# Kernel optimization log

Measured on AMD Instinct MI355X. Metric: run time of the kernel, lower is better.

## Reference

```python
import jax, jax.numpy as jnp
import numpy as np

N_NODES, N_EDGES, D, N_MOVIE, N_GENRE, L_MAX = 50000, 400000, 128, 20400, 30, 680
HOPS, HEADS, C_HEAD, N_LAYERS, T_HEADS, FF = 3, 4, 32, 4, 4, 2048


def _leaky(x, s):
    return jnp.where(x >= 0, x, s * x)


def _layer_norm(x, g, b, eps=1e-5):
    m = x.mean(-1, keepdims=True)
    v = ((x - m) ** 2).mean(-1, keepdims=True)
    return (x - m) / jnp.sqrt(v + eps) * g + b


def _gat_conv(x, ei, W, a_src, a_dst, b):
    # PyG GATConv: add self-loops, per-head linear, edge-softmax over incoming edges.
    N = x.shape[0]
    loop = jnp.arange(N)
    src = jnp.concatenate([ei[0], loop])
    dst = jnp.concatenate([ei[1], loop])
    h = (x @ W.T).reshape(N, HEADS, C_HEAD)
    al_s = (h * a_src[None]).sum(-1)  # [N, H]
    al_d = (h * a_dst[None]).sum(-1)
    e = _leaky(al_s[src] + al_d[dst], 0.2)  # [E+N, H]
    m = jax.ops.segment_max(e, dst, num_segments=N)
    ee = jnp.exp(e - m[dst])
    den = jax.ops.segment_sum(ee, dst, num_segments=N)
    alpha = ee / den[dst]
    out = jax.ops.segment_sum(h[src] * alpha[:, :, None], dst, num_segments=N)
    return out.reshape(N, HEADS * C_HEAD) + b


def _mha(y, pad_mask, qkv_w, qkv_b, out_w, out_b):
    B, S, Dm = y.shape
    hd = Dm // T_HEADS
    qkv = y @ qkv_w.T + qkv_b
    q, k, v = jnp.split(qkv, 3, axis=-1)
    q = q.reshape(B, S, T_HEADS, hd).transpose(0, 2, 1, 3)
    k = k.reshape(B, S, T_HEADS, hd).transpose(0, 2, 1, 3)
    v = v.reshape(B, S, T_HEADS, hd).transpose(0, 2, 1, 3)
    scores = jnp.einsum('bhqd,bhkd->bhqk', q, k) / jnp.sqrt(jnp.float32(hd))
    scores = jnp.where(pad_mask[:, None, None, :], -1e9, scores)
    a = jax.nn.softmax(scores, axis=-1)
    o = jnp.einsum('bhqk,bhkd->bhqd', a, v).transpose(0, 2, 1, 3).reshape(B, S, Dm)
    return o @ out_w.T + out_b


def _forward(x, e0, e1, e2, movie_idx, genre, gat_W, gat_att_src, gat_att_dst, gat_bias,
             dec_W, dec_b, qkv_w, qkv_b, out_w, out_b, ln1_g, ln1_b, ln2_g, ln2_b,
             ffn_w1, ffn_b1, ffn_w2, ffn_b2, fus_w, fus_b):
    edges = [e0, e1, e2]
    acc = jnp.zeros_like(x)
    for kk in range(HOPS):  # multi-hop GAT with exp hop decay (dropout off: eval)
        h = _gat_conv(x, edges[kk], gat_W[kk], gat_att_src[kk], gat_att_dst[kk], gat_bias[kk])
        h = _leaky(h @ dec_W[kk].T + dec_b[kk], 0.01)
        acc = acc + float(np.exp(-0.1 * kk)) * h
    x = acc
    xm = x[movie_idx]  # x[genre_mask]
    # group movie nodes into padded per-genre sequences [N_GENRE, L_MAX, D]
    onehot = jax.nn.one_hot(genre, N_GENRE, dtype=jnp.int32)
    pos = jnp.cumsum(onehot, axis=0)[jnp.arange(genre.shape[0]), genre] - 1
    counts = jnp.sum(onehot, axis=0)
    all_genre = jnp.zeros((N_GENRE, L_MAX, x.shape[1]), x.dtype).at[genre, pos].set(xm)
    pad_mask = jnp.arange(L_MAX)[None, :] >= counts[:, None]  # True = padding
    y = all_genre
    for l in range(N_LAYERS):  # PyTorch post-LN TransformerEncoder, relu FFN, eval dropout
        a = _mha(y, pad_mask, qkv_w[l], qkv_b[l], out_w[l], out_b[l])
        y = _layer_norm(y + a, ln1_g[l], ln1_b[l])
        f = jax.nn.relu(y @ ffn_w1[l].T + ffn_b1[l]) @ ffn_w2[l].T + ffn_b2[l]
        y = _layer_norm(y + f, ln2_g[l], ln2_b[l])
    # genre_backward: mean-pool per genre, gather back per node
    valid = (~pad_mask).astype(x.dtype)
    pooled = (y * valid[..., None]).sum(1) / jnp.maximum(valid.sum(1), 1.0)[:, None]
    emb = pooled[genre]
    fused = _leaky(jnp.concatenate([xm, emb], axis=1) @ fus_w.T + fus_b, 0.01)
    return x.at[movie_idx].set(fused)


def setup_inputs() -> dict:
    key = jax.random.key(0)
    ks = jax.random.split(key, 24)
    s = 0.05
    nrm = lambda i, shp: jax.random.normal(ks[i], shp, jnp.float32) * s
    return {
        'x': jax.random.normal(ks[0], (N_NODES, D), jnp.float32),
        'edge_index_hop0': jax.random.randint(ks[1], (2, N_EDGES), 0, N_NODES),
        'edge_index_hop1': jax.random.randint(ks[2], (2, N_EDGES), 0, N_NODES),
        'edge_index_hop2': jax.random.randint(ks[3], (2, N_EDGES), 0, N_NODES),
        'movie_idx': jnp.arange(N_MOVIE),
        'genre': jnp.arange(N_MOVIE) % N_GENRE,
        'gat_W': nrm(4, (HOPS, D, D)),
        'gat_att_src': nrm(5, (HOPS, HEADS, C_HEAD)),
        'gat_att_dst': nrm(6, (HOPS, HEADS, C_HEAD)),
        'gat_bias': nrm(7, (HOPS, D)),
        'dec_W': nrm(8, (HOPS, D, D)),
        'dec_b': nrm(9, (HOPS, D)),
        'qkv_w': nrm(10, (N_LAYERS, 3 * D, D)),
        'qkv_b': nrm(11, (N_LAYERS, 3 * D)),
        'out_w': nrm(12, (N_LAYERS, D, D)),
        'out_b': nrm(13, (N_LAYERS, D)),
        'ln1_g': jnp.ones((N_LAYERS, D), jnp.float32),
        'ln1_b': jnp.zeros((N_LAYERS, D), jnp.float32),
        'ln2_g': jnp.ones((N_LAYERS, D), jnp.float32),
        'ln2_b': jnp.zeros((N_LAYERS, D), jnp.float32),
        'ffn_w1': nrm(14, (N_LAYERS, FF, D)),
        'ffn_b1': nrm(15, (N_LAYERS, FF)),
        'ffn_w2': nrm(16, (N_LAYERS, D, FF)),
        'ffn_b2': nrm(17, (N_LAYERS, D)),
        'fus_w': nrm(18, (D, 2 * D)),
        'fus_b': nrm(19, (D,)),
    }


def reference(x, edge_index_hop0, edge_index_hop1, edge_index_hop2, movie_idx, genre,
              gat_W, gat_att_src, gat_att_dst, gat_bias, dec_W, dec_b,
              qkv_w, qkv_b, out_w, out_b, ln1_g, ln1_b, ln2_g, ln2_b,
              ffn_w1, ffn_b1, ffn_w2, ffn_b2, fus_w, fus_b):
    return _forward(x, edge_index_hop0, edge_index_hop1, edge_index_hop2, movie_idx, genre,
                    gat_W, gat_att_src, gat_att_dst, gat_bias, dec_W, dec_b,
                    qkv_w, qkv_b, out_w, out_b, ln1_g, ln1_b, ln2_g, ln2_b,
                    ffn_w1, ffn_b1, ffn_w2, ffn_b2, fus_w, fus_b)
```

## Files before the change

### kernel.cpp

```cpp
#include <hip/hip_runtime.h>

#define N_NODES  50000
#define N_EDGES  400000
#define DIM      128
#define N_MOVIE  20400
#define N_GENRE  30
#define L_MAX    680
#define NROWS    (N_GENRE * L_MAX)
#define FF       2048
#define N_LAYERS 4

#define NBKT 98
#define NPB  512
#define ECAP 4608
#define SCAP 5120
#define EPGB (NBKT * ECAP)
#define SPGB (NBKT * SCAP)

typedef __attribute__((ext_vector_type(8))) short bf16x8;
typedef __attribute__((ext_vector_type(4))) float f32x4;

#define MFMA16 __builtin_amdgcn_mfma_f32_16x16x32_bf16

__device__ __forceinline__ float b2f(ushort u) {
    union { unsigned i; float f; } c; c.i = ((unsigned)u) << 16; return c.f;
}
__device__ __forceinline__ ushort f2b(float f) {
    union { float f; unsigned i; } c; c.f = f;
    unsigned u = c.i;
    u += 0x7FFFu + ((u >> 16) & 1u);
    return (ushort)(u >> 16);
}
__device__ __forceinline__ bf16x8 load8s(const ushort* p) {
    return *(const bf16x8*)p;
}
__device__ __forceinline__ void async16(const ushort* g, ushort* l) {
    __builtin_amdgcn_global_load_lds(
        (const __attribute__((address_space(1))) void*)g,
        (__attribute__((address_space(3))) void*)l, 16, 0, 0);
}

__device__ __forceinline__ void cvt8(const float* s, ushort* d, int i) {
    const float4* q = (const float4*)(s + (size_t)i * 8);
    float4 a = q[0], b = q[1];
    bf16x8 r;
    r[0] = (short)f2b(a.x); r[1] = (short)f2b(a.y);
    r[2] = (short)f2b(a.z); r[3] = (short)f2b(a.w);
    r[4] = (short)f2b(b.x); r[5] = (short)f2b(b.y);
    r[6] = (short)f2b(b.z); r[7] = (short)f2b(b.w);
    *(bf16x8*)(d + (size_t)i * 8) = r;
}

__global__ void cvt32(const float* __restrict__ s, ushort* __restrict__ d, int n8)
{
    int i = blockIdx.x * blockDim.x + threadIdx.x;
    if (i < n8) cvt8(s, d, i);
}

__global__ void cvt_w(const float* gatW, const float* decW, const float* qkvW,
                      const float* outW, const float* fw1, const float* fw2,
                      const float* fusW,
                      ushort* gatWb, ushort* decWb, ushort* qkvWb,
                      ushort* outWb, ushort* fw1b, ushort* fw2b, ushort* fusWb)
{
    const float* s; ushort* d; int n8;
    switch (blockIdx.y) {
        case 0: s = gatW; d = gatWb; n8 = 49152 / 8; break;
        case 1: s = decW; d = decWb; n8 = 49152 / 8; break;
        case 2: s = qkvW; d = qkvWb; n8 = 196608 / 8; break;
        case 3: s = outW; d = outWb; n8 = 65536 / 8; break;
        case 4: s = fw1;  d = fw1b;  n8 = 1048576 / 8; break;
        case 5: s = fw2;  d = fw2b;  n8 = 1048576 / 8; break;
        default: s = fusW; d = fusWb; n8 = 32768 / 8; break;
    }
    int i = blockIdx.x * 256 + threadIdx.x;
    if (i < n8) cvt8(s, d, i);
}

template<int BM, int ACT, int EPI, int OBF>
__global__ __launch_bounds__(256) void gemm_lds(
    const ushort* __restrict__ A, const ushort* __restrict__ W,
    const float* __restrict__ bias, void* __restrict__ Cv,
    int M, int N, int K, float scale)
{
    __shared__ ushort smem[BM * 128 + 128 * 128];
    ushort* As = smem;
    ushort* Ws = smem + BM * 128;
    const int tid  = threadIdx.x;
    const int wave = tid >> 6, lane = tid & 63;
    const int quad = lane >> 4, l16 = lane & 15;
    const int m0 = blockIdx.x * BM;
    const int n0 = blockIdx.y * 128;

    constexpr int MT = BM / 32;
    const int mbase = (wave & 1) * (BM / 2);
    const int nbase = (wave >> 1) * 64;

    f32x4 acc[MT][4] = {};
    for (int k0 = 0; k0 < K; k0 += 128) {
        if (k0) __syncthreads();
#pragma unroll
        for (int i = 0; i < BM / 16; i++) {
            int seg = i * 256 + tid;
            int r = seg >> 4, s = seg & 15;
            int rg = min(m0 + r, M - 1);
            async16(A + (size_t)rg * K + k0 + ((s ^ (r & 15)) * 8),
                    As + r * 128 + s * 8);
        }
#pragma unroll
        for (int i = 0; i < 8; i++) {
            int seg = i * 256 + tid;
            int r = seg >> 4, s = seg & 15;
            async16(W + (size_t)(n0 + r) * K + k0 + ((s ^ (r & 15)) * 8),
                    Ws + r * 128 + s * 8);
        }
        __syncthreads();

#pragma unroll
        for (int kk = 0; kk < 4; kk++) {
            bf16x8 a[MT], b[4];
#pragma unroll
            for (int mt = 0; mt < MT; mt++)
                a[mt] = load8s(As + (mbase + mt * 16 + l16) * 128 +
                               (((kk * 4 + quad) ^ l16) * 8));
#pragma unroll
            for (int nt = 0; nt < 4; nt++)
                b[nt] = load8s(Ws + (nbase + nt * 16 + l16) * 128 +
                               (((kk * 4 + quad) ^ l16) * 8));
#pragma unroll
            for (int mt = 0; mt < MT; mt++)
#pragma unroll
                for (int nt = 0; nt < 4; nt++)
                    acc[mt][nt] = MFMA16(a[mt], b[nt], acc[mt][nt], 0, 0, 0);
        }
    }

    if constexpr (OBF == 1) {
        static_assert(BM == 128, "OBF=1 staged epilogue assumes BM=128");
        ushort* Cs = smem;
        __syncthreads();
#pragma unroll
        for (int p = 0; p < 2; p++) {
            if ((wave & 1) == p) {
#pragma unroll
                for (int nt = 0; nt < 4; nt++) {
                    const int col = nbase + nt * 16 + l16;
                    const float bv = bias ? bias[n0 + col] : 0.f;
#pragma unroll
                    for (int mt = 0; mt < MT; mt++) {
                        const int rl = mt * 16 + quad * 4;
#pragma unroll
                        for (int r = 0; r < 4; r++) {
                            float v = acc[mt][nt][r] + bv;
                            if (ACT == 1) v = (v >= 0.f) ? v : 0.01f * v;
                            if (ACT == 2) v = fmaxf(v, 0.f);
                            Cs[(rl + r) * 128 + col] = f2b(v);
                        }
                    }
                }
            }
            __syncthreads();
            const int row = tid >> 2, cb = (tid & 3) * 32;
            const int grow = m0 + p * 64 + row;
            if (grow < M) {
                const ushort* s = Cs + row * 128 + cb;
                ushort* dp = (ushort*)Cv + (size_t)grow * N + n0 + cb;
                *(int4*)(dp)      = *(const int4*)(s);
                *(int4*)(dp + 8)  = *(const int4*)(s + 8);
                *(int4*)(dp + 16) = *(const int4*)(s + 16);
                *(int4*)(dp + 24) = *(const int4*)(s + 24);
            }
            __syncthreads();
        }
    } else {
#pragma unroll
        for (int nt = 0; nt < 4; nt++) {
            const int col = n0 + nbase + nt * 16 + l16;
            const float bv = bias ? bias[col] : 0.f;
#pragma unroll
            for (int mt = 0; mt < MT; mt++) {
                if (OBF == 2) {
                    const int row0 = m0 + mbase + mt * 16 + quad * 4;
                    if (row0 < M) {
                        ushort4 pk;
                        pk.x = f2b(acc[mt][nt][0] + bv);
                        pk.y = f2b(acc[mt][nt][1] + bv);
                        pk.z = f2b(acc[mt][nt][2] + bv);
                        pk.w = f2b(acc[mt][nt][3] + bv);
                        *(ushort4*)((ushort*)Cv + (size_t)col * M + row0) = pk;
                    }
                } else {
#pragma unroll
                    for (int r = 0; r < 4; r++) {
                        const int row = m0 + mbase + mt * 16 + quad * 4 + r;
                        if (row < M) {
                            float v = acc[mt][nt][r] + bv;
                            if (ACT == 1) v = (v >= 0.f) ? v : 0.01f * v;
                            if (ACT == 2) v = fmaxf(v, 0.f);
                            const size_t idx = (size_t)row * N + col;
                            if (EPI == 1) ((float*)Cv)[idx] += scale * v;
                            else          ((float*)Cv)[idx] = v;
                        }
                    }
                }
            }
        }
    }
}

__global__ __launch_bounds__(256, 2) void ffn_fused(
    const ushort* __restrict__ y, const ushort* __restrict__ w1,
    const float* __restrict__ b1, const ushort* __restrict__ w2,
    const float* __restrict__ b2,
    float* __restrict__ o0, float* __restrict__ o1,
    float* __restrict__ o2, float* __restrict__ o3, int M)
{
    __shared__ ushort f1s[2][32 * 128];
    __shared__ ushort f2s[2][128 * 32];
    __shared__ ushort mids[4][32 * 40];

    const int tid  = threadIdx.x;
    const int wave = tid >> 6, lane = tid & 63;
    const int quad = lane >> 4, l16 = lane & 15;
    const int m0 = blockIdx.x * 128;
    const int fh = blockIdx.y;
    const int fbase = fh * (FF / 4);
    float* o = (fh == 0) ? o0 : (fh == 1) ? o1 : (fh == 2) ? o2 : o3;

    const int sw1 = ((tid & 15) ^ (tid >> 4)) * 8;
    const int sw2 = ((tid & 3) ^ ((tid >> 3) & 3)) * 8;

    const int wrow = m0 + wave * 32;
    bf16x8 yf[2][4];
#pragma unroll
    for (int mt = 0; mt < 2; mt++) {
        const int mr = min(wrow + mt * 16 + l16, M - 1);
#pragma unroll
        for (int ks = 0; ks < 4; ks++)
            yf[mt][ks] = load8s(y + (size_t)mr * 128 + ks * 32 + quad * 8);
    }

#pragma unroll
    for (int i = 0; i < 2; i++) {
        int row = i * 16 + (tid >> 4);
        async16(w1 + (size_t)(fbase + row) * 128 + sw1,
                f1s[0] + row * 128 + (tid & 15) * 8);
    }
#pragma unroll
    for (int i = 0; i < 2; i++) {
        int row = i * 64 + (tid >> 2);
        async16(w2 + (size_t)row * FF + fbase + sw2,
                f2s[0] + row * 32 + (tid & 3) * 8);
    }

    f32x4 oacc[2][8] = {};
    ushort* midw = mids[wave];
    int cur = 0;
    __syncthreads();

    for (int fo = 0; fo < FF / 4; fo += 32) {
        if (fo + 32 < FF / 4) {
            const int fn = fbase + fo + 32;
#pragma unroll
            for (int i = 0; i < 2; i++) {
                int row = i * 16 + (tid >> 4);
                async16(w1 + (size_t)(fn + row) * 128 + sw1,
                        f1s[cur ^ 1] + row * 128 + (tid & 15) * 8);
            }
#pragma unroll
            for (int i = 0; i < 2; i++) {
                int row = i * 64 + (tid >> 2);
                async16(w2 + (size_t)row * FF + fn + sw2,
                        f2s[cur ^ 1] + row * 32 + (tid & 3) * 8);
            }
        }
        const ushort* F1 = f1s[cur];
        const ushort* F2 = f2s[cur];

        f32x4 midacc[2][2] = {};
#pragma unroll
        for (int ks = 0; ks < 4; ks++) {
            const int csA = (((ks * 4 + quad) ^ l16) & 15) * 8;
#pragma unroll
            for (int ft = 0; ft < 2; ft++) {
                bf16x8 wf = load8s(F1 + (ft * 16 + l16) * 128 + csA);
                midacc[0][ft] = MFMA16(wf, yf[0][ks], midacc[0][ft], 0, 0, 0);
                midacc[1][ft] = MFMA16(wf, yf[1][ks], midacc[1][ft], 0, 0, 0);
            }
        }
#pragma unroll
        for (int mt = 0; mt < 2; mt++)
#pragma unroll
            for (int ft = 0; ft < 2; ft++) {
                const float4 bb = *(const float4*)(b1 + fbase + fo + ft * 16 + quad * 4);
                ushort4 pk;
                pk.x = f2b(fmaxf(midacc[mt][ft][0] + bb.x, 0.f));
                pk.y = f2b(fmaxf(midacc[mt][ft][1] + bb.y, 0.f));
                pk.z = f2b(fmaxf(midacc[mt][ft][2] + bb.z, 0.f));
                pk.w = f2b(fmaxf(midacc[mt][ft][3] + bb.w, 0.f));
                *(ushort4*)(midw + (mt * 16 + l16) * 40 + ft * 16 + quad * 4) = pk;
            }
        bf16x8 mf0 = load8s(midw + (size_t)l16 * 40 + quad * 8);
        bf16x8 mf1 = load8s(midw + (size_t)(16 + l16) * 40 + quad * 8);
        const int gB = (quad ^ ((l16 >> 1) & 3)) * 8;
#pragma unroll
        for (int dt = 0; dt < 8; dt++) {
            bf16x8 wf = load8s(F2 + (dt * 16 + l16) * 32 + gB);
            oacc[0][dt] = MFMA16(wf, mf0, oacc[0][dt], 0, 0, 0);
            oacc[1][dt] = MFMA16(wf, mf1, oacc[1][dt], 0, 0, 0);
        }
        __syncthreads();
        cur ^= 1;
    }

#pragma unroll
    for (int mt = 0; mt < 2; mt++) {
        const int m = wrow + mt * 16 + l16;
        if (m < M) {
            float* op = o + (size_t)m * 128 + quad * 4;
#pragma unroll
            for (int dt = 0; dt < 8; dt++) {
                float4 v;
                if (fh == 0) {
                    const float4 bv = *(const float4*)(b2 + dt * 16 + quad * 4);
                    v.x = oacc[mt][dt][0] + bv.x;
                    v.y = oacc[mt][dt][1] + bv.y;
                    v.z = oacc[mt][dt][2] + bv.z;
                    v.w = oacc[mt][dt][3] + bv.w;
                } else {
                    v.x = oacc[mt][dt][0];
                    v.y = oacc[mt][dt][1];
                    v.z = oacc[mt][dt][2];
                    v.w = oacc[mt][dt][3];
                }
                *(float4*)(op + dt * 16) = v;
            }
        }
    }
}

__global__ void gat_al(const ushort* __restrict__ h,
                       const float* __restrict__ asrc, const float* __restrict__ adst,
                       float* __restrict__ als, float* __restrict__ ald, int N)
{
    int idx = blockIdx.x * blockDim.x + threadIdx.x;
    if (idx >= N * 4) return;
    int n = idx >> 2, hh = idx & 3;
    const ushort* hp = h + (size_t)n * DIM + hh * 32;
    float s = 0.f, d = 0.f;
#pragma unroll
    for (int q = 0; q < 4; q++) {
        bf16x8 hv = load8s(hp + q * 8);
#pragma unroll
        for (int c = 0; c < 8; c++) {
            float v = b2f((ushort)hv[c]);
            s += v * asrc[hh * 32 + q * 8 + c];
            d += v * adst[hh * 32 + q * 8 + c];
        }
    }
    als[idx] = s; ald[idx] = d;
}

__global__ void csr_initb(int* __restrict__ bcur)
{
    int i = blockIdx.x * 256 + threadIdx.x;
    if (i < 3 * NBKT) bcur[i * 16] = (i % NBKT) * ECAP;
}

__global__ __launch_bounds__(256) void csr_route(
    const int* __restrict__ e0, const int* __restrict__ e1, const int* __restrict__ e2,
    int* __restrict__ bcur, int* __restrict__ ebuf)
{
    __shared__ int hist[NBKT], base[NBKT], cur[NBKT];
    const int g = blockIdx.y, t = threadIdx.x;
    const int* e = (g == 0) ? e0 : (g == 1) ? e1 : e2;
    const int i0 = blockIdx.x * 4096;
    for (int j = t; j < NBKT; j += 256) { hist[j] = 0; cur[j] = 0; }
    __syncthreads();
    unsigned pk[16]; int bk[16];
#pragma unroll
    for (int j = 0; j < 16; j++) {
        int i = i0 + j * 256 + t;
        if (i < N_EDGES) {
            int s = e[i], d = e[N_EDGES + i];
            bk[j] = d >> 9;
            pk[j] = (unsigned)s | ((unsigned)(d & 511) << 16);
            atomicAdd(&hist[bk[j]], 1);
        } else bk[j] = -1;
    }
    __syncthreads();
    for (int j = t; j < NBKT; j += 256)
        if (hist[j]) base[j] = atomicAdd(&bcur[(g * NBKT + j) * 16], hist[j]);
    __syncthreads();
#pragma unroll
    for (int j = 0; j < 16; j++)
        if (bk[j] >= 0) {
            int p = base[bk[j]] + atomicAdd(&cur[bk[j]], 1);
            ebuf[(size_t)g * EPGB + p] = (int)pk[j];
        }
}

__global__ __launch_bounds__(256) void csr_build(
    const int* __restrict__ bcur, const int* __restrict__ ebuf,
    int* __restrict__ off, int* __restrict__ deg, int* __restrict__ srcs)
{
    __shared__ int hist[NPB];
    __shared__ int part[256];
    const int g = blockIdx.y, b = blockIdx.x, t = threadIdx.x;
    const int nb0 = b * NPB;
    const int nn = min(NPB, N_NODES - nb0);
    const int cnt = bcur[(g * NBKT + b) * 16] - b * ECAP;
    const int* eb = ebuf + (size_t)g * EPGB + b * ECAP;

    for (int j = t; j < NPB; j += 256) hist[j] = (j < nn) ? 1 : 0;
    __syncthreads();
    for (int i = t; i < cnt; i += 256)
        atomicAdd(&hist[(eb[i] >> 16) & 511], 1);
    __syncthreads();

    int a0 = hist[t * 2], a1 = hist[t * 2 + 1];
    int sum = a0 + a1;
    part[t] = sum;
    __syncthreads();
    for (int d = 1; d < 256; d <<= 1) {
        int x = (t >= d) ? part[t - d] : 0;
        __syncthreads();
        part[t] += x;
        __syncthreads();
    }
    const int excl = part[t] - sum;
    __syncthreads();
    const int sb = b * SCAP;
    hist[t * 2]     = excl;
    hist[t * 2 + 1] = excl + a0;
    if (t * 2 < nn) {
        off[(size_t)g * N_NODES + nb0 + t * 2] = sb + excl;
        deg[(size_t)g * N_NODES + nb0 + t * 2] = a0;
    }
    if (t * 2 + 1 < nn) {
        off[(size_t)g * N_NODES + nb0 + t * 2 + 1] = sb + excl + a0;
        deg[(size_t)g * N_NODES + nb0 + t * 2 + 1] = a1;
    }
    __syncthreads();

    int* sg = srcs + (size_t)g * SPGB + sb;
    for (int i = t; i < cnt; i += 256) {
        int v = eb[i];
        int p = atomicAdd(&hist[(v >> 16) & 511], 1);
        sg[p] = v & 0xFFFF;
    }
    for (int j = t; j < nn; j += 256) {
        int p = atomicAdd(&hist[j], 1);
        sg[p] = nb0 + j;
    }
}

__global__ __launch_bounds__(256) void gat_gather(
    const int* __restrict__ off, const int* __restrict__ deg, const int* __restrict__ srcs,
    const ushort* __restrict__ hb, const float* __restrict__ als,
    const float* __restrict__ ald, const float* __restrict__ bias,
    ushort* __restrict__ ob)
{
    int w = (blockIdx.x * 256 + threadIdx.x) >> 6;
    int lane = threadIdx.x & 63;
    if (w >= N_NODES) return;
    const int grp  = lane >> 4;
    const int l16  = lane & 15;
    const int head = l16 >> 2;
    const float adv = ald[(size_t)w * 4 + head];
    const int jb = off[w], dg = deg[w];

    float acc[8] = {};
    float wsum = 0.f;

    int j = grp;
    int s = (j < dg) ? srcs[jb + j] : 0;
    while (j < dg) {
        const int jn = j + 4;
        const int sn = (jn < dg) ? srcs[jb + jn] : 0;
        bf16x8 hv = load8s(hb + (size_t)s * DIM + l16 * 8);
        float e = als[(size_t)s * 4 + head] + adv;
        e = (e >= 0.f) ? e : 0.2f * e;
        const float wg = __expf(e);
        wsum += wg;
#pragma unroll
        for (int c = 0; c < 8; c++) acc[c] += wg * b2f((ushort)hv[c]);
        j = jn; s = sn;
    }

    wsum += __shfl_xor(wsum, 16, 64);
    wsum += __shfl_xor(wsum, 32, 64);
#pragma unroll
    for (int c = 0; c < 8; c++) {
        acc[c] += __shfl_xor(acc[c], 16, 64);
        acc[c] += __shfl_xor(acc[c], 32, 64);
    }

    if (grp == 0) {
        const float inv = 1.f / wsum;
        bf16x8 r;
#pragma unroll
        for (int c = 0; c < 8; c++)
            r[c] = (short)f2b(acc[c] * inv + bias[l16 * 8 + c]);
        *(bf16x8*)(ob + (size_t)w * DIM + l16 * 8) = r;
    }
}

__global__ void calc_pos(const int* __restrict__ genre, int* __restrict__ pos,
                         int* __restrict__ cnt, int NM)
{
    int i = blockIdx.x * blockDim.x + threadIdx.x;
    if (i < NM) pos[i] = atomicAdd(&cnt[genre[i]], 1);
}

__global__ void build_y(const float* __restrict__ acc, const int* __restrict__ midx,
                        const int* __restrict__ genre, const int* __restrict__ pos,
                        float* __restrict__ y, ushort* __restrict__ yb)
{
    int i = blockIdx.x, c = threadIdx.x;
    int g = genre[i], p = pos[i];
    float v = acc[(size_t)midx[i] * DIM + c];
    size_t o = ((size_t)g * L_MAX + p) * DIM + c;
    y[o] = v; yb[o] = f2b(v);
}

#define SP 40

__global__ __launch_bounds__(256) void flash_attn(
    const ushort* __restrict__ qk, const ushort* __restrict__ vtg,
    const int* __restrict__ cnt, ushort* __restrict__ o)
{
    __shared__ ushort Pb[4][32 * SP];

    const int qt = blockIdx.x, hh = blockIdx.y, g = blockIdx.z;
    const int t = threadIdx.x, wave = t >> 6, lane = t & 63;
    const int quad = lane >> 4, l16 = lane & 15;
    const int L = cnt[g];
    const float scale = 0.17677669529663687f;
    const ushort* base = qk + (size_t)g * L_MAX * 256;
    const ushort* vb0 = vtg + (size_t)(hh * 32 + l16) * NROWS + g * L_MAX;
    const ushort* vb1 = vb0 + (size_t)16 * NROWS;

    const int q0 = qt * 128 + wave * 32;
    bf16x8 a0 = load8s(base + (size_t)min(q0 + l16,      L_MAX - 1) * 256 + hh * 32 + quad * 8);
    bf16x8 a1 = load8s(base + (size_t)min(q0 + 16 + l16, L_MAX - 1) * 256 + hh * 32 + quad * 8);

    f32x4 oacc[2][2] = {};
    float rsum[2] = {0.f, 0.f};
    ushort* P = Pb[wave];

    for (int kt = 0; kt < 704; kt += 32) {
        bf16x8 b0 = load8s(base + (size_t)min(kt + l16,      L_MAX - 1) * 256 + 128 + hh * 32 + quad * 8);
        bf16x8 b1 = load8s(base + (size_t)min(kt + 16 + l16, L_MAX - 1) * 256 + 128 + hh * 32 + quad * 8);
        f32x4 z = {};
        f32x4 st00 = MFMA16(b0, a0, z, 0, 0, 0);
        f32x4 st01 = MFMA16(b0, a1, z, 0, 0, 0);
        f32x4 st10 = MFMA16(b1, a0, z, 0, 0, 0);
        f32x4 st11 = MFMA16(b1, a1, z, 0, 0, 0);

        const int kc0 = kt + quad * 4, kc1 = kt + 16 + quad * 4;
#pragma unroll
        for (int qh = 0; qh < 2; qh++) {
            const f32x4 sA = qh ? st01 : st00;
            const f32x4 sB = qh ? st11 : st10;
            float w[8];
#pragma unroll
            for (int r = 0; r < 4; r++) {
                w[r]     = (kc0 + r < L) ? __expf(sA[r] * scale) : 0.f;
                w[4 + r] = (kc1 + r < L) ? __expf(sB[r] * scale) : 0.f;
                rsum[qh] += w[r] + w[4 + r];
            }
            ushort4 pk0, pk1;
            pk0.x = f2b(w[0]); pk0.y = f2b(w[1]); pk0.z = f2b(w[2]); pk0.w = f2b(w[3]);
            pk1.x = f2b(w[4]); pk1.y = f2b(w[5]); pk1.z = f2b(w[6]); pk1.w = f2b(w[7]);
            *(ushort4*)(P + (qh * 16 + l16) * SP + quad * 4)      = pk0;
            *(ushort4*)(P + (qh * 16 + l16) * SP + 16 + quad * 4) = pk1;
        }
        bf16x8 p0 = load8s(P + (size_t)l16 * SP + quad * 8);
        bf16x8 p1 = load8s(P + (size_t)(16 + l16) * SP + quad * 8);
        bf16x8 v0 = load8s(vb0 + kt + quad * 8);
        bf16x8 v1 = load8s(vb1 + kt + quad * 8);
        oacc[0][0] = MFMA16(v0, p0, oacc[0][0], 0, 0, 0);
        oacc[0][1] = MFMA16(v0, p1, oacc[0][1], 0, 0, 0);
        oacc[1][0] = MFMA16(v1, p0, oacc[1][0], 0, 0, 0);
        oacc[1][1] = MFMA16(v1, p1, oacc[1][1], 0, 0, 0);
    }

#pragma unroll
    for (int qh = 0; qh < 2; qh++) {
        float s = rsum[qh];
        s += __shfl_xor(s, 16, 64);
        s += __shfl_xor(s, 32, 64);
        const int q = q0 + qh * 16 + l16;
        if (q < L_MAX) {
            const float inv = 1.f / s;
#pragma unroll
            for (int dh = 0; dh < 2; dh++) {
                ushort4 pk;
                pk.x = f2b(oacc[dh][qh][0] * inv);
                pk.y = f2b(oacc[dh][qh][1] * inv);
                pk.z = f2b(oacc[dh][qh][2] * inv);
                pk.w = f2b(oacc[dh][qh][3] * inv);
                *(ushort4*)(o + ((size_t)(g * L_MAX + q)) * DIM + hh * 32 + dh * 16 + quad * 4) = pk;
            }
        }
    }
}

__global__ __launch_bounds__(256) void ln_res(
    float* __restrict__ y, const float* __restrict__ res,
    const float* __restrict__ res2, const float* __restrict__ res3,
    const float* __restrict__ res4,
    const float* __restrict__ g, const float* __restrict__ b,
    ushort* __restrict__ yb)
{
    const int r = blockIdx.x * 4 + (threadIdx.x >> 6);
    const int lane = threadIdx.x & 63;
    const size_t base = (size_t)r * DIM + lane * 2;
    float2 v = *(const float2*)(y + base);
    {
        float2 a = *(const float2*)(res + base);
        v.x += a.x; v.y += a.y;
    }
    if (res2) {
        float2 a = *(const float2*)(res2 + base);
        v.x += a.x; v.y += a.y;
    }
    if (res3) {
        float2 a = *(const float2*)(res3 + base);
        float2 c = *(const float2*)(res4 + base);
        v.x += a.x + c.x; v.y += a.y + c.y;
    }
    float s = v.x + v.y;
#pragma unroll
    for (int off = 32; off; off >>= 1) s += __shfl_xor(s, off, 64);
    const float mean = s * (1.f / 128.f);
    const float dx = v.x - mean, dy = v.y - mean;
    float q = dx * dx + dy * dy;
#pragma unroll
    for (int off = 32; off; off >>= 1) q += __shfl_xor(q, off, 64);
    const float rst = rsqrtf(q * (1.f / 128.f) + 1e-5f);
    const float2 gg = *(const float2*)(g + lane * 2);
    const float2 bb = *(const float2*)(b + lane * 2);
    float2 ov;
    ov.x = dx * rst * gg.x + bb.x;
    ov.y = dy * rst * gg.y + bb.y;
    *(float2*)(y + base) = ov;
    ushort2 pk;
    pk.x = f2b(ov.x);
    pk.y = f2b(ov.y);
    *(ushort2*)(yb + base) = pk;
}

__global__ __launch_bounds__(256) void pool_partial(
    const float* __restrict__ y, const int* __restrict__ cnt, float* __restrict__ pooled)
{
    __shared__ float sh[128];
    const int g = blockIdx.x, seg = blockIdx.y, t = threadIdx.x;
    const int c = t & 127, h = t >> 7;
    const int L = cnt[g];
    const int k0 = seg * 40, k1 = min(k0 + 40, L);
    float s = 0.f;
    for (int k = k0 + h; k < k1; k += 2) s += y[((size_t)g * L_MAX + k) * DIM + c];
    if (h) sh[c] = s;
    __syncthreads();
    if (!h) {
        float tot = s + sh[c];
        if (k0 < L) atomicAdd(&pooled[g * DIM + c], tot / (float)max(L, 1));
    }
}

__global__ void build_fin(const float* __restrict__ acc, const float* __restrict__ pooled,
                          const int* __restrict__ midx, const int* __restrict__ genre,
                          ushort* __restrict__ A2)
{
    const int i = blockIdx.x, t = threadIdx.x;
    float v = (t < 128) ? acc[(size_t)midx[i] * DIM + t]
                        : pooled[genre[i] * DIM + (t - 128)];
    A2[(size_t)i * 256 + t] = f2b(v);
}

__global__ void scatter_movies(const float* __restrict__ fused, const int* __restrict__ midx,
                               float* __restrict__ out)
{
    const int i = blockIdx.x, c = threadIdx.x;
    out[(size_t)midx[i] * DIM + c] = fused[(size_t)i * DIM + c];
}

extern "C" void kernel_launch(void* const* d_in, const int* in_sizes, int n_in,
                              void* d_out, int out_size, void* d_ws, size_t ws_size,
                              hipStream_t stream)
{
    const float* x      = (const float*)d_in[0];
    const int* e[3]     = { (const int*)d_in[1], (const int*)d_in[2], (const int*)d_in[3] };
    const int* midx     = (const int*)d_in[4];
    const int* genre    = (const int*)d_in[5];
    const float* gatW   = (const float*)d_in[6];
    const float* attS   = (const float*)d_in[7];
    const float* attD   = (const float*)d_in[8];
    const float* gatB   = (const float*)d_in[9];
    const float* decW   = (const float*)d_in[10];
    const float* decB   = (const float*)d_in[11];
    const float* qkvW   = (const float*)d_in[12];
    const float* qkvB   = (const float*)d_in[13];
    const float* outW   = (const float*)d_in[14];
    const float* outB   = (const float*)d_in[15];
    const float* ln1g   = (const float*)d_in[16];
    const float* ln1b   = (const float*)d_in[17];
    const float* ln2g   = (const float*)d_in[18];
    const float* ln2b   = (const float*)d_in[19];
    const float* fw1    = (const float*)d_in[20];
    const float* fb1    = (const float*)d_in[21];
    const float* fw2    = (const float*)d_in[22];
    const float* fb2    = (const float*)d_in[23];
    const float* fusW   = (const float*)d_in[24];
    const float* fusB   = (const float*)d_in[25];
    float* out = (float*)d_out;

    float* ws  = (float*)d_ws;
    float* acc = ws;
    float* R   = ws + 6400000;
    ushort* xb   = (ushort*)(R);
    ushort* hb   = (ushort*)(R + 3200000);
    ushort* gbx  = (ushort*)(R + 6400000);
    float*  als  = R + 9600000;
    float*  ald  = R + 9800000;
    int*   bcur  = (int*)(R + 10000000);
    int*   ebuf  = (int*)(R + 10004736);
    int*   off3  = (int*)(R + 11359488);
    int*   deg3  = (int*)(R + 11509488);
    int*   srcs3 = (int*)(R + 11659488);
    ushort* gatWb= (ushort*)(R + 13164768);
    ushort* decWb= (ushort*)(R + 13189344);
    float*  ybuf  = R;
    float*  tmp   = R + 2611200;
    ushort* ybx   = (ushort*)(R + 5222400);
    ushort* attnb = (ushort*)(R + 6528000);
    ushort* qkvb  = (ushort*)(R + 7833600);
    ushort* vtg   = (ushort*)(R + 10444800);
    ushort* finb  = (ushort*)(R + 11750400);
    float*  tmp2  = R + 14361600;
    float*  tmp3  = R + 16972800;
    float*  tmp4  = R + 19584000;
    float*  pooled= R + 22195200;
    int*    cntb  = (int*)(R + 22199040);
    int*    posb  = cntb + 32;
    ushort* qkvWb = (ushort*)(R + 22220000);
    ushort* outWb = (ushort*)(R + 22318304);
    ushort* fw1b  = (ushort*)(R + 22351072);
    ushort* fw2b  = (ushort*)(R + 22875360);
    ushort* fusWb = (ushort*)(R + 23399648);

    const float decay[3] = { 1.0f, 0.90483741803595952f, 0.81873075307798182f };

    cvt_w<<<dim3(512, 7), 256, 0, stream>>>(
        gatW, decW, qkvW, outW, fw1, fw2, fusW,
        gatWb, decWb, qkvWb, outWb, fw1b, fw2b, fusWb);
    cvt32<<<(6400000 / 8 + 255) / 256, 256, 0, stream>>>(x, xb, 6400000 / 8);

    csr_initb<<<(3 * NBKT + 255) / 256, 256, 0, stream>>>(bcur);
    csr_route<<<dim3((N_EDGES + 4095) / 4096, 3), 256, 0, stream>>>(
        e[0], e[1], e[2], bcur, ebuf);
    csr_build<<<dim3(NBKT, 3), 256, 0, stream>>>(bcur, ebuf, off3, deg3, srcs3);

    for (int k = 0; k < 3; k++) {
        gemm_lds<128, 0, 0, 1><<<dim3(391, 1), 256, 0, stream>>>(
            xb, gatWb + k * DIM * DIM, nullptr, hb, N_NODES, DIM, DIM, 1.f);
        gat_al<<<(N_NODES * 4 + 255) / 256, 256, 0, stream>>>(
            hb, attS + k * DIM, attD + k * DIM, als, ald, N_NODES);
        gat_gather<<<(N_NODES * 64 + 255) / 256, 256, 0, stream>>>(
            off3 + (size_t)k * N_NODES, deg3 + (size_t)k * N_NODES,
            srcs3 + (size_t)k * SPGB, hb, als, ald, gatB + k * DIM, gbx);
        if (k == 0)
            gemm_lds<128, 1, 0, 0><<<dim3(391, 1), 256, 0, stream>>>(
                gbx, decWb, decB, acc, N_NODES, DIM, DIM, 1.f);
        else
            gemm_lds<128, 1, 1, 0><<<dim3(391, 1), 256, 0, stream>>>(
                gbx, decWb + k * DIM * DIM, decB + k * DIM, acc, N_NODES, DIM, DIM, decay[k]);
    }

    hipMemsetAsync(cntb, 0, 32 * 4, stream);
    calc_pos<<<(N_MOVIE + 255) / 256, 256, 0, stream>>>(genre, posb, cntb, N_MOVIE);
    build_y<<<N_MOVIE, 128, 0, stream>>>(acc, midx, genre, posb, ybuf, ybx);

    for (int l = 0; l < N_LAYERS; l++) {
        gemm_lds<128, 0, 0, 1><<<dim3(160, 2), 256, 0, stream>>>(
            ybx, qkvWb + (size_t)l * 384 * DIM, qkvB + l * 384, qkvb, NROWS, 256, DIM, 1.f);
        gemm_lds<128, 0, 0, 2><<<dim3(160, 1), 256, 0, stream>>>(
            ybx, qkvWb + (size_t)l * 384 * DIM + 256 * DIM, qkvB + l * 384 + 256,
            vtg, NROWS, DIM, DIM, 1.f);
        flash_attn<<<dim3(6, 4, 30), 256, 0, stream>>>(qkvb, vtg, cntb, attnb);
        gemm_lds<64, 0, 0, 0><<<dim3(319, 1), 256, 0, stream>>>(
            attnb, outWb + (size_t)l * DIM * DIM, outB + l * DIM, tmp, NROWS, DIM, DIM, 1.f);
        ln_res<<<NROWS / 4, 256, 0, stream>>>(ybuf, tmp, nullptr, nullptr, nullptr,
                                              ln1g + l * DIM, ln1b + l * DIM, ybx);
        ffn_fused<<<dim3((NROWS + 127) / 128, 4), 256, 0, stream>>>(
            ybx, fw1b + (size_t)l * FF * DIM, fb1 + (size_t)l * FF,
            fw2b + (size_t)l * DIM * FF, fb2 + (size_t)l * DIM,
            tmp, tmp2, tmp3, tmp4, NROWS);
        ln_res<<<NROWS / 4, 256, 0, stream>>>(ybuf, tmp, tmp2, tmp3, tmp4,
                                              ln2g + l * DIM, ln2b + l * DIM, ybx);
    }

    hipMemsetAsync(pooled, 0, 3840 * 4, stream);
    pool_partial<<<dim3(N_GENRE, 17), 256, 0, stream>>>(ybuf, cntb, pooled);
    build_fin<<<N_MOVIE, 256, 0, stream>>>(acc, pooled, midx, genre, finb);
    gemm_lds<64, 1, 0, 0><<<dim3(319, 1), 256, 0, stream>>>(
        finb, fusWb, fusB, tmp, NROWS, DIM, 256, 1.f);

    hipMemcpyAsync(out, acc, (size_t)6400000 * 4, hipMemcpyDeviceToDevice, stream);
    scatter_movies<<<N_MOVIE, 128, 0, stream>>>(tmp, midx, out);
}
```

Before: 922.5 us.

## Batch GAT hops across grid z, fuse QKV GEMMs, accumulate directly into output

The three GAT hops' projection GEMM, attention-logit and gather kernels now each run as one launch indexed by blockIdx, with per-hop buffers, so small kernels fill the GPU better and launch count drops. The separate QK and V GEMMs become a single qkv_gemm launch with three column blocks. The accumulator is written straight into the output buffer, removing a 25.6MB device-to-device copy. The cost is larger workspace for per-hop buffers, and the final scatter now depends on acc aliasing out.

Result: faster. 867.0 us (-6.0%).

```diff
diff --git a/kernel.cpp b/kernel.cpp
--- a/kernel.cpp
+++ b/kernel.cpp
@@ -79,9 +79,9 @@
 
 template<int BM, int ACT, int EPI, int OBF>
 __global__ __launch_bounds__(256) void gemm_lds(
-    const ushort* __restrict__ A, const ushort* __restrict__ W,
+    const ushort* __restrict__ A, const ushort* __restrict__ W_,
     const float* __restrict__ bias, void* __restrict__ Cv,
-    int M, int N, int K, float scale)
+    int M, int N, int K, float scale, size_t wstride, size_t cstride)
 {
     __shared__ ushort smem[BM * 128 + 128 * 128];
     ushort* As = smem;
@@ -91,6 +91,8 @@
     const int quad = lane >> 4, l16 = lane & 15;
     const int m0 = blockIdx.x * BM;
     const int n0 = blockIdx.y * 128;
+    const int hop = blockIdx.z;
+    const ushort* W = W_ + (size_t)hop * wstride;
 
     constexpr int MT = BM / 32;
     const int mbase = (wave & 1) * (BM / 2);
@@ -164,7 +166,8 @@
             const int grow = m0 + p * 64 + row;
             if (grow < M) {
                 const ushort* s = Cs + row * 128 + cb;
-                ushort* dp = (ushort*)Cv + (size_t)grow * N + n0 + cb;
+                ushort* dp = (ushort*)Cv + (size_t)hop * cstride +
+                             (size_t)grow * N + n0 + cb;
                 *(int4*)(dp)      = *(const int4*)(s);
                 *(int4*)(dp + 8)  = *(const int4*)(s + 8);
                 *(int4*)(dp + 16) = *(const int4*)(s + 16);
@@ -179,29 +182,120 @@
             const float bv = bias ? bias[col] : 0.f;
 #pragma unroll
             for (int mt = 0; mt < MT; mt++) {
-                if (OBF == 2) {
-                    const int row0 = m0 + mbase + mt * 16 + quad * 4;
-                    if (row0 < M) {
-                        ushort4 pk;
-                        pk.x = f2b(acc[mt][nt][0] + bv);
-                        pk.y = f2b(acc[mt][nt][1] + bv);
-                        pk.z = f2b(acc[mt][nt][2] + bv);
-                        pk.w = f2b(acc[mt][nt][3] + bv);
-                        *(ushort4*)((ushort*)Cv + (size_t)col * M + row0) = pk;
+#pragma unroll
+                for (int r = 0; r < 4; r++) {
+                    const int row = m0 + mbase + mt * 16 + quad * 4 + r;
+                    if (row < M) {
+                        float v = acc[mt][nt][r] + bv;
+                        if (ACT == 1) v = (v >= 0.f) ? v : 0.01f * v;
+                        if (ACT == 2) v = fmaxf(v, 0.f);
+                        const size_t idx = (size_t)row * N + col;
+                        if (EPI == 1) ((float*)Cv)[idx] += scale * v;
+                        else          ((float*)Cv)[idx] = v;
                     }
-                } else {
-#pragma unroll
-                    for (int r = 0; r < 4; r++) {
-                        const int row = m0 + mbase + mt * 16 + quad * 4 + r;
-                        if (row < M) {
-                            float v = acc[mt][nt][r] + bv;
-                            if (ACT == 1) v = (v >= 0.f) ? v : 0.01f * v;
-                            if (ACT == 2) v = fmaxf(v, 0.f);
-                            const size_t idx = (size_t)row * N + col;
-                            if (EPI == 1) ((float*)Cv)[idx] += scale * v;
-                            else          ((float*)Cv)[idx] = v;
-                        }
+                }
+            }
+        }
+    }
+}
+
+__global__ __launch_bounds__(256) void qkv_gemm(
+    const ushort* __restrict__ A, const ushort* __restrict__ W0,
+    const float* __restrict__ bias0, ushort* __restrict__ qkv,
+    ushort* __restrict__ vt, int M)
+{
+    __shared__ ushort smem[2 * 128 * 128];
+    ushort* As = smem;
+    ushort* Ws = smem + 128 * 128;
+    const int tid  = threadIdx.x;
+    const int wave = tid >> 6, lane = tid & 63;
+    const int quad = lane >> 4, l16 = lane & 15;
+    const int m0 = blockIdx.x * 128;
+    const int sel = blockIdx.y;
+    const ushort* W = W0 + (size_t)sel * 128 * 128;
+    const int mbase = (wave & 1) * 64;
+    const int nbase = (wave >> 1) * 64;
+
+    f32x4 acc[4][4] = {};
+#pragma unroll
+    for (int i = 0; i < 8; i++) {
+        int seg = i * 256 + tid;
+        int r = seg >> 4, s = seg & 15;
+        int rg = min(m0 + r, M - 1);
+        async16(A + (size_t)rg * 128 + ((s ^ (r & 15)) * 8), As + r * 128 + s * 8);
+    }
+#pragma unroll
+    for (int i = 0; i < 8; i++) {
+        int seg = i * 256 + tid;
+        int r = seg >> 4, s = seg & 15;
+        async16(W + (size_t)r * 128 + ((s ^ (r & 15)) * 8), Ws + r * 128 + s * 8);
+    }
+    __syncthreads();
+#pragma unroll
+    for (int kk = 0; kk < 4; kk++) {
+        bf16x8 a[4], b[4];
+#pragma unroll
+        for (int mt = 0; mt < 4; mt++)
+            a[mt] = load8s(As + (mbase + mt * 16 + l16) * 128 +
+                           (((kk * 4 + quad) ^ l16) * 8));
+#pragma unroll
+        for (int nt = 0; nt < 4; nt++)
+            b[nt] = load8s(Ws + (nbase + nt * 16 + l16) * 128 +
+                           (((kk * 4 + quad) ^ l16) * 8));
+#pragma unroll
+        for (int mt = 0; mt < 4; mt++)
+#pragma unroll
+            for (int nt = 0; nt < 4; nt++)
+                acc[mt][nt] = MFMA16(a[mt], b[nt], acc[mt][nt], 0, 0, 0);
+    }
+
+    if (sel < 2) {
+        ushort* Cs = smem;
+        __syncthreads();
+#pragma unroll
+        for (int p = 0; p < 2; p++) {
+            if ((wave & 1) == p) {
+#pragma unroll
+                for (int nt = 0; nt < 4; nt++) {
+                    const int col = nbase + nt * 16 + l16;
+                    const float bv = bias0[sel * 128 + col];
+#pragma unroll
+                    for (int mt = 0; mt < 4; mt++) {
+                        const int rl = mt * 16 + quad * 4;
+#pragma unroll
+                        for (int r = 0; r < 4; r++)
+                            Cs[(rl + r) * 128 + col] = f2b(acc[mt][nt][r] + bv);
                     }
+                }
+            }
+            __syncthreads();
+            const int row = tid >> 2, cb = (tid & 3) * 32;
+            const int grow = m0 + p * 64 + row;
+            if (grow < M) {
+                const ushort* s = Cs + row * 128 + cb;
+                ushort* dp = qkv + (size_t)grow * 256 + sel * 128 + cb;
+                *(int4*)(dp)      = *(const int4*)(s);
+                *(int4*)(dp + 8)  = *(const int4*)(s + 8);
+                *(int4*)(dp + 16) = *(const int4*)(s + 16);
+                *(int4*)(dp + 24) = *(const int4*)(s + 24);
+            }
+            __syncthreads();
+        }
+    } else {
+#pragma unroll
+        for (int nt = 0; nt < 4; nt++) {
+            const int col = nbase + nt * 16 + l16;
+            const float bv = bias0[256 + col];
+#pragma unroll
+            for (int mt = 0; mt < 4; mt++) {
+                const int row0 = m0 + mbase + mt * 16 + quad * 4;
+                if (row0 < M) {
+                    ushort4 pk;
+                    pk.x = f2b(acc[mt][nt][0] + bv);
+                    pk.y = f2b(acc[mt][nt][1] + bv);
+                    pk.z = f2b(acc[mt][nt][2] + bv);
+                    pk.w = f2b(acc[mt][nt][3] + bv);
+                    *(ushort4*)(vt + (size_t)col * M + row0) = pk;
                 }
             }
         }
@@ -218,7 +312,6 @@
     __shared__ ushort f1s[2][32 * 128];
     __shared__ ushort f2s[2][128 * 32];
     __shared__ ushort mids[4][32 * 40];
-
     const int tid  = threadIdx.x;
     const int wave = tid >> 6, lane = tid & 63;
     const int quad = lane >> 4, l16 = lane & 15;
@@ -339,12 +432,16 @@
     }
 }
 
-__global__ void gat_al(const ushort* __restrict__ h,
+__global__ void gat_al(const ushort* __restrict__ hb3,
                        const float* __restrict__ asrc, const float* __restrict__ adst,
-                       float* __restrict__ als, float* __restrict__ ald, int N)
+                       float* __restrict__ als3, float* __restrict__ ald3, int N)
 {
     int idx = blockIdx.x * blockDim.x + threadIdx.x;
     if (idx >= N * 4) return;
+    const int hop = blockIdx.y;
+    const ushort* h = hb3 + (size_t)hop * N * DIM;
+    const float* as_ = asrc + hop * DIM;
+    const float* ad_ = adst + hop * DIM;
     int n = idx >> 2, hh = idx & 3;
     const ushort* hp = h + (size_t)n * DIM + hh * 32;
     float s = 0.f, d = 0.f;
@@ -354,11 +451,12 @@
 #pragma unroll
         for (int c = 0; c < 8; c++) {
             float v = b2f((ushort)hv[c]);
-            s += v * asrc[hh * 32 + q * 8 + c];
-            d += v * adst[hh * 32 + q * 8 + c];
-        }
-    }
-    als[idx] = s; ald[idx] = d;
+            s += v * as_[hh * 32 + q * 8 + c];
+            d += v * ad_[hh * 32 + q * 8 + c];
+        }
+    }
+    als3[(size_t)hop * N * 4 + idx] = s;
+    ald3[(size_t)hop * N * 4 + idx] = d;
 }
 
 __global__ void csr_initb(int* __restrict__ bcur)
@@ -456,14 +554,24 @@
 }
 
 __global__ __launch_bounds__(256) void gat_gather(
-    const int* __restrict__ off, const int* __restrict__ deg, const int* __restrict__ srcs,
-    const ushort* __restrict__ hb, const float* __restrict__ als,
-    const float* __restrict__ ald, const float* __restrict__ bias,
-    ushort* __restrict__ ob)
+    const int* __restrict__ off3, const int* __restrict__ deg3,
+    const int* __restrict__ srcs3, const ushort* __restrict__ hb3,
+    const float* __restrict__ als3, const float* __restrict__ ald3,
+    const float* __restrict__ bias3, ushort* __restrict__ gbx3)
 {
     int w = (blockIdx.x * 256 + threadIdx.x) >> 6;
     int lane = threadIdx.x & 63;
     if (w >= N_NODES) return;
+    const int hop = blockIdx.y;
+    const int* off = off3 + (size_t)hop * N_NODES;
+    const int* deg = deg3 + (size_t)hop * N_NODES;
+    const int* srcs = srcs3 + (size_t)hop * SPGB;
+    const ushort* hb = hb3 + (size_t)hop * N_NODES * DIM;
+    const float* als = als3 + (size_t)hop * N_NODES * 4;
+    const float* ald = ald3 + (size_t)hop * N_NODES * 4;
+    const float* bias = bias3 + hop * DIM;
+    ushort* ob = gbx3 + (size_t)hop * N_NODES * DIM;
+
     const int grp  = lane >> 4;
     const int l16  = lane & 15;
     const int head = l16 >> 2;
@@ -718,20 +826,20 @@
     float* out = (float*)d_out;
 
     float* ws  = (float*)d_ws;
-    float* acc = ws;
+    float* acc = out;
     float* R   = ws + 6400000;
-    ushort* xb   = (ushort*)(R);
-    ushort* hb   = (ushort*)(R + 3200000);
-    ushort* gbx  = (ushort*)(R + 6400000);
-    float*  als  = R + 9600000;
-    float*  ald  = R + 9800000;
-    int*   bcur  = (int*)(R + 10000000);
-    int*   ebuf  = (int*)(R + 10004736);
-    int*   off3  = (int*)(R + 11359488);
-    int*   deg3  = (int*)(R + 11509488);
-    int*   srcs3 = (int*)(R + 11659488);
-    ushort* gatWb= (ushort*)(R + 13164768);
-    ushort* decWb= (ushort*)(R + 13189344);
+    ushort* xb   = (ushort*)(ws);
+    ushort* gatWb= (ushort*)(ws + 3200000);
+    ushort* decWb= (ushort*)(ws + 3224576);
+    float*  als3 = ws + 3249152;
+    float*  ald3 = ws + 3849152;
+    int*    off3 = (int*)(ws + 4449152);
+    int*    deg3 = (int*)(ws + 4599152);
+    ushort* hb3  = (ushort*)(R);
+    ushort* gbx3 = (ushort*)(R + 9600000);
+    int*   bcur  = (int*)(R + 19200000);
+    int*   ebuf  = (int*)(R + 19204736);
+    int*   srcs3 = (int*)(R + 20559488);
     float*  ybuf  = R;
     float*  tmp   = R + 2611200;
     ushort* ybx   = (ushort*)(R + 5222400);
@@ -763,20 +871,21 @@
         e[0], e[1], e[2], bcur, ebuf);
     csr_build<<<dim3(NBKT, 3), 256, 0, stream>>>(bcur, ebuf, off3, deg3, srcs3);
 
+    gemm_lds<128, 0, 0, 1><<<dim3(391, 1, 3), 256, 0, stream>>>(
+        xb, gatWb, nullptr, hb3, N_NODES, DIM, DIM, 1.f,
+        (size_t)DIM * DIM, (size_t)N_NODES * DIM);
+    gat_al<<<dim3((N_NODES * 4 + 255) / 256, 3), 256, 0, stream>>>(
+        hb3, attS, attD, als3, ald3, N_NODES);
+    gat_gather<<<dim3(N_NODES * 64 / 256, 3), 256, 0, stream>>>(
+        off3, deg3, srcs3, hb3, als3, ald3, gatB, gbx3);
     for (int k = 0; k < 3; k++) {
-        gemm_lds<128, 0, 0, 1><<<dim3(391, 1), 256, 0, stream>>>(
-            xb, gatWb + k * DIM * DIM, nullptr, hb, N_NODES, DIM, DIM, 1.f);
-        gat_al<<<(N_NODES * 4 + 255) / 256, 256, 0, stream>>>(
-            hb, attS + k * DIM, attD + k * DIM, als, ald, N_NODES);
-        gat_gather<<<(N_NODES * 64 + 255) / 256, 256, 0, stream>>>(
-            off3 + (size_t)k * N_NODES, deg3 + (size_t)k * N_NODES,
-            srcs3 + (size_t)k * SPGB, hb, als, ald, gatB + k * DIM, gbx);
         if (k == 0)
-            gemm_lds<128, 1, 0, 0><<<dim3(391, 1), 256, 0, stream>>>(
-                gbx, decWb, decB, acc, N_NODES, DIM, DIM, 1.f);
+            gemm_lds<128, 1, 0, 0><<<dim3(391, 1, 1), 256, 0, stream>>>(
+                gbx3, decWb, decB, acc, N_NODES, DIM, DIM, 1.f, 0, 0);
         else
-            gemm_lds<128, 1, 1, 0><<<dim3(391, 1), 256, 0, stream>>>(
-                gbx, decWb + k * DIM * DIM, decB + k * DIM, acc, N_NODES, DIM, DIM, decay[k]);
+            gemm_lds<128, 1, 1, 0><<<dim3(391, 1, 1), 256, 0, stream>>>(
+                gbx3 + (size_t)k * N_NODES * DIM, decWb + k * DIM * DIM,
+                decB + k * DIM, acc, N_NODES, DIM, DIM, decay[k], 0, 0);
     }
 
     hipMemsetAsync(cntb, 0, 32 * 4, stream);
@@ -784,14 +893,12 @@
     build_y<<<N_MOVIE, 128, 0, stream>>>(acc, midx, genre, posb, ybuf, ybx);
 
     for (int l = 0; l < N_LAYERS; l++) {
-        gemm_lds<128, 0, 0, 1><<<dim3(160, 2), 256, 0, stream>>>(
-            ybx, qkvWb + (size_t)l * 384 * DIM, qkvB + l * 384, qkvb, NROWS, 256, DIM, 1.f);
-        gemm_lds<128, 0, 0, 2><<<dim3(160, 1), 256, 0, stream>>>(
-            ybx, qkvWb + (size_t)l * 384 * DIM + 256 * DIM, qkvB + l * 384 + 256,
-            vtg, NROWS, DIM, DIM, 1.f);
+        qkv_gemm<<<dim3(160, 3), 256, 0, stream>>>(
+            ybx, qkvWb + (size_t)l * 384 * DIM, qkvB + l * 384, qkvb, vtg, NROWS);
         flash_attn<<<dim3(6, 4, 30), 256, 0, stream>>>(qkvb, vtg, cntb, attnb);
-        gemm_lds<64, 0, 0, 0><<<dim3(319, 1), 256, 0, stream>>>(
-            attnb, outWb + (size_t)l * DIM * DIM, outB + l * DIM, tmp, NROWS, DIM, DIM, 1.f);
+        gemm_lds<64, 0, 0, 0><<<dim3(319, 1, 1), 256, 0, stream>>>(
+            attnb, outWb + (size_t)l * DIM * DIM, outB + l * DIM, tmp,
+            NROWS, DIM, DIM, 1.f, 0, 0);
         ln_res<<<NROWS / 4, 256, 0, stream>>>(ybuf, tmp, nullptr, nullptr, nullptr,
                                               ln1g + l * DIM, ln1b + l * DIM, ybx);
         ffn_fused<<<dim3((NROWS + 127) / 128, 4), 256, 0, stream>>>(
@@ -805,9 +912,8 @@
     hipMemsetAsync(pooled, 0, 3840 * 4, stream);
     pool_partial<<<dim3(N_GENRE, 17), 256, 0, stream>>>(ybuf, cntb, pooled);
     build_fin<<<N_MOVIE, 256, 0, stream>>>(acc, pooled, midx, genre, finb);
-    gemm_lds<64, 1, 0, 0><<<dim3(319, 1), 256, 0, stream>>>(
-        finb, fusWb, fusB, tmp, NROWS, DIM, 256, 1.f);
-
-    hipMemcpyAsync(out, acc, (size_t)6400000 * 4, hipMemcpyDeviceToDevice, stream);
+    gemm_lds<64, 1, 0, 0><<<dim3(319, 1, 1), 256, 0, stream>>>(
+        finb, fusWb, fusB, tmp, NROWS, DIM, 256, 1.f, 0, 0);
+
     scatter_movies<<<N_MOVIE, 128, 0, stream>>>(tmp, midx, out);
 }
```
